# Kernel tuning notes

Hardware: AMD Instinct MI355X
Metric: run time of the kernel (lower is better)

## Reference

```python
import jax, jax.numpy as jnp
import numpy as np

RADIUS = 3.0  # suppression radius in meters (init kwarg `radius`)


def _radius_nms(x, y, valid, radius):
    """Greedy radius NMS over points in index order.
    x, y: [N] coordinates; valid: [N] bool (point belongs to this class).
    Returns keep mask [N]: point kept iff valid and not within `radius` of
    any previously kept point.
    """
    N = x.shape[0]
    r2 = radius * radius

    def step(supp, i):
        keep = valid[i] & jnp.logical_not(supp[i])
        d2 = (x - x[i]) ** 2 + (y - y[i]) ** 2  # [N]
        supp = supp | (keep & (d2 <= r2))
        return supp, keep

    _, keeps = jax.lax.scan(step, jnp.zeros(N, dtype=bool), jnp.arange(N))
    return keeps


def setup_inputs() -> dict:
    key = jax.random.key(0)
    k1, k2 = jax.random.split(key)
    B, C, W, H, CL = 4, 4, 64, 128, 5
    segmented_channels = jax.random.normal(k1, (B, C, W, H), dtype=jnp.float32)
    # lidar channels 0,1 are x,y point coordinates (meters); scale for realism
    lidar = jax.random.normal(k2, (B, CL, W, H), dtype=jnp.float32) * 30.0
    return {"segmented_channels": segmented_channels, "lidar": lidar}


def reference(segmented_channels, lidar):
    B, C, W, H = segmented_channels.shape
    N = W * H
    # val, ind = segmented_channels.max(dim=1) -> per-pixel predicted class
    ind = jnp.argmax(segmented_channels, axis=1).reshape(B, N)  # [B, N] int
    x = lidar[:, 0].reshape(B, N)  # [B, N]
    y = lidar[:, 1].reshape(B, N)
    # classes 1 .. C-1 (class 0 = background, skipped in the loop)
    classes = jnp.arange(1, C)
    valid = ind[:, None, :] == classes[None, :, None]  # [B, C-1, N] bool
    # vmap greedy NMS over classes, then over batch (x,y shared across classes)
    nms_c = jax.vmap(_radius_nms, in_axes=(None, None, 0, None))
    nms_bc = jax.vmap(nms_c, in_axes=(0, 0, 0, None))
    keep = nms_bc(x, y, valid, RADIUS)  # [B, C-1, N] bool
    # dense (padded) stand-in for the ragged per-class kept point lists:
    # kept coordinates where keep, zeros elsewhere
    coords = jnp.stack([x, y], axis=-1)  # [B, N, 2]
    kept_coords = coords[:, None, :, :] * keep[..., None].astype(coords.dtype)  # [B, C-1, N, 2]
    return kept_coords, keep
```

## Files before the change

kernel.cpp:

```cpp
#include <hip/hip_runtime.h>
#include <cstdint>


#define NPTS 8192
#define CAP  2304
#define R2C  9.0f
#define GW   56
#define GORG 117.6f
#define GINV 0.23809524f
#define GMAXC 55.0f
#define SENT 3.0e37f

#define WS_STRIDE 32768
#define WS_XY     0
#define WS_CELL   18432
#define WS_OIDX   23040
#define WS_KEPT   27648
#define WS_M      27936
#define WS_NEED   (12 * WS_STRIDE)

__global__ __launch_bounds__(1024) void k1_prep(
    const float* __restrict__ seg,
    const float* __restrict__ lidar,
    float* __restrict__ out,
    char* __restrict__ ws)
{
#pragma clang fp contract(off)
    const int blk = blockIdx.x;
    const int tid = threadIdx.x;
    if (blk >= 12) {
        ((float4*)out)[(size_t)(blk - 12) * 1024 + tid] =
            make_float4(0.f, 0.f, 0.f, 0.f);
        return;
    }
    const int b    = blk / 3;
    const int cls  = (blk % 3) + 1;
    const int lane = tid & 63;
    const int wv   = tid >> 6;
    __shared__ int waveTot[16];

    const float* segb = seg + (size_t)b * 4 * NPTS;
    const float* lx   = lidar + (size_t)b * 5 * NPTS;
    const float* ly   = lx + NPTS;

    const int n0 = tid * 8;
    const float4 a0 = *(const float4*)(segb + n0);
    const float4 a1 = *(const float4*)(segb + n0 + 4);
    const float4 b0 = *(const float4*)(segb + NPTS + n0);
    const float4 b1 = *(const float4*)(segb + NPTS + n0 + 4);
    const float4 c0 = *(const float4*)(segb + 2 * NPTS + n0);
    const float4 c1 = *(const float4*)(segb + 2 * NPTS + n0 + 4);
    const float4 d0 = *(const float4*)(segb + 3 * NPTS + n0);
    const float4 d1 = *(const float4*)(segb + 3 * NPTS + n0 + 4);
    const float4 xv0 = *(const float4*)(lx + n0);
    const float4 xv1 = *(const float4*)(lx + n0 + 4);
    const float4 yv0 = *(const float4*)(ly + n0);
    const float4 yv1 = *(const float4*)(ly + n0 + 4);

    const float v0[8] = {a0.x,a0.y,a0.z,a0.w, a1.x,a1.y,a1.z,a1.w};
    const float v1[8] = {b0.x,b0.y,b0.z,b0.w, b1.x,b1.y,b1.z,b1.w};
    const float v2[8] = {c0.x,c0.y,c0.z,c0.w, c1.x,c1.y,c1.z,c1.w};
    const float v3[8] = {d0.x,d0.y,d0.z,d0.w, d1.x,d1.y,d1.z,d1.w};
    const float px[8] = {xv0.x,xv0.y,xv0.z,xv0.w, xv1.x,xv1.y,xv1.z,xv1.w};
    const float py[8] = {yv0.x,yv0.y,yv0.z,yv0.w, yv1.x,yv1.y,yv1.z,yv1.w};

    int flags = 0, cnt = 0;
#pragma unroll
    for (int k = 0; k < 8; ++k) {
        int bi = 0; float bv = v0[k];
        if (v1[k] > bv) { bv = v1[k]; bi = 1; }
        if (v2[k] > bv) { bv = v2[k]; bi = 2; }
        if (v3[k] > bv) { bv = v3[k]; bi = 3; }
        if (bi == cls) { flags |= (1 << k); ++cnt; }
    }

    int v = cnt;
    for (int off = 1; off < 64; off <<= 1) {
        int nv = __shfl_up(v, off, 64);
        if (lane >= off) v += nv;
    }
    if (lane == 63) waveTot[wv] = v;
    __syncthreads();
    if (wv == 0) {
        int t = (lane < 16) ? waveTot[lane] : 0;
        for (int off = 1; off < 16; off <<= 1) {
            int nt = __shfl_up(t, off, 64);
            if (lane >= off) t += nt;
        }
        if (lane < 16) waveTot[lane] = t;
    }
    __syncthreads();

    int M = waveTot[15];
    if (M > CAP) M = CAP;

    char* wsp = ws + (size_t)blk * WS_STRIDE;
    float2* wxy = (float2*)(wsp + WS_XY);
    unsigned short* wcell = (unsigned short*)(wsp + WS_CELL);
    unsigned short* woidx = (unsigned short*)(wsp + WS_OIDX);
    if (tid == 0) *(int*)(wsp + WS_M) = M;

    int base = ((wv == 0) ? 0 : waveTot[wv - 1]) + v - cnt;
#pragma unroll
    for (int k = 0; k < 8; ++k) {
        if (flags & (1 << k)) {
            if (base < CAP) {
                wxy[base] = make_float2(px[k], py[k]);
                float fx = floorf((px[k] + GORG) * GINV);
                fx = fminf(fmaxf(fx, 0.0f), GMAXC);
                float fy = floorf((py[k] + GORG) * GINV);
                fy = fminf(fmaxf(fy, 0.0f), GMAXC);
                wcell[base] = (unsigned short)(((int)fy << 8) | (int)fx);
                woidx[base] = (unsigned short)(n0 + k);
            }
            ++base;
        }
    }
}

__global__ __launch_bounds__(64) void k2_nms(char* __restrict__ ws)
{
#pragma clang fp contract(off)
    const int p    = blockIdx.x;
    const int lane = threadIdx.x;

    char* wsp = ws + (size_t)p * WS_STRIDE;
    const float2* wxy = (const float2*)(wsp + WS_XY);
    const unsigned short* wcell = (const unsigned short*)(wsp + WS_CELL);
    unsigned long long* wkept = (unsigned long long*)(wsp + WS_KEPT);
    const int M = *(const int*)(wsp + WS_M);

    __shared__ float2 gslot[GW * GW * 4];
    __shared__ unsigned int cnt32[(GW * GW + 3) / 4];

    const float4 s4 = make_float4(SENT, SENT, SENT, SENT);
    float4* g4 = (float4*)gslot;
    for (int i = lane; i < GW * GW * 2; i += 64) g4[i] = s4;
    for (int i = lane; i < (GW * GW + 3) / 4; i += 64) cnt32[i] = 0u;

    const int ntiles = (M + 63) >> 6;
    const int packSent = (55 << 8) | 55;

    float qx = 3.0e38f, qy = 3.0e38f;
    int cc = packSent;
    if (lane < M) {
        float2 q = wxy[lane]; qx = q.x; qy = q.y;
        cc = wcell[lane];
    }

    for (int t = 0; t < ntiles; ++t) {
        const int ts = t << 6;

        float qxN = 3.0e38f, qyN = 3.0e38f;
        int ccN = packSent;
        {
            const int p2 = ts + 64 + lane;
            if (p2 < M) {
                float2 q = wxy[p2]; qxN = q.x; qyN = q.y;
                ccN = wcell[p2];
            }
        }

        const int cx = cc & 0xFF, cy = cc >> 8;
        const int cxm = (cx > 0) ? cx - 1 : 0;
        const int cxp = (cx < GW - 1) ? cx + 1 : GW - 1;
        const int rm  = ((cy > 0) ? cy - 1 : 0) * GW;
        const int r0  = cy * GW;
        const int rp  = ((cy < GW - 1) ? cy + 1 : GW - 1) * GW;
        const int cLin = r0 + cx;
        const int c9[9] = { rm + cxm, rm + cx, rm + cxp,
                            r0 + cxm, cLin,    r0 + cxp,
                            rp + cxm, rp + cx, rp + cxp };

        float mm = 1.0e30f;
#pragma unroll
        for (int i = 0; i < 9; ++i) {
            const int sb = c9[i] * 4;
            const float2 s0 = gslot[sb];
            const float2 s1 = gslot[sb + 1];
            const float2 s2r = gslot[sb + 2];
            const float2 s3 = gslot[sb + 3];
            float dx, dy;
            dx = qx - s0.x; dy = qy - s0.y; const float e0 = dx * dx + dy * dy;
            dx = qx - s1.x; dy = qy - s1.y; const float e1 = dx * dx + dy * dy;
            dx = qx - s2r.x; dy = qy - s2r.y; const float e2 = dx * dx + dy * dy;
            dx = qx - s3.x; dy = qy - s3.y; const float e3 = dx * dx + dy * dy;
            const float cm = fminf(fminf(e0, e1), fminf(e2, e3));
            mm = fminf(mm, cm);
        }
        const bool sup = (mm <= R2C);

        int cntT = M - ts; if (cntT > 64) cntT = 64;
        const unsigned long long tm =
            (cntT >= 64) ? ~0ull : ((1ull << cntT) - 1ull);
        unsigned long long alive = __ballot(!sup) & tm;
        unsigned long long keepm = 0ull;
        while (alive) {
            const int l = __builtin_ctzll(alive);
            const float xl = __int_as_float(
                __builtin_amdgcn_readlane(__float_as_int(qx), l));
            const float yl = __int_as_float(
                __builtin_amdgcn_readlane(__float_as_int(qy), l));
            const float dx = qx - xl;
            const float dy = qy - yl;
            unsigned long long b2 = __ballot((dx * dx + dy * dy) <= R2C);
            keepm |= (1ull << l);
            alive &= ~b2;
        }
        if (lane == 0) wkept[t] = keepm;

        if ((keepm >> lane) & 1ull) {
            const unsigned sh = 8u * (unsigned)(cLin & 3);
            unsigned old = atomicAdd(&cnt32[cLin >> 2], 1u << sh);
            unsigned mc = (old >> sh) & 0xFFu;
            if (mc < 4u) gslot[cLin * 4 + (int)mc] = make_float2(qx, qy);
        }

        qx = qxN; qy = qyN; cc = ccN;
    }
}

__global__ __launch_bounds__(1024) void k3_scatter(
    float* __restrict__ out, const char* __restrict__ ws)
{
    const int p   = blockIdx.x;
    const int tid = threadIdx.x;
    const char* wsp = ws + (size_t)p * WS_STRIDE;
    const float2* wxy = (const float2*)(wsp + WS_XY);
    const unsigned short* woidx = (const unsigned short*)(wsp + WS_OIDX);
    const unsigned long long* wkept =
        (const unsigned long long*)(wsp + WS_KEPT);
    const int M = *(const int*)(wsp + WS_M);

    float* out0 = out + (size_t)p * NPTS * 2;
    float* out1 = out + 196608 + (size_t)p * NPTS;
    for (int j = tid; j < M; j += 1024) {
        if ((wkept[j >> 6] >> (j & 63)) & 1ull) {
            const int n = woidx[j];
            float2 q = wxy[j];
            out0[2 * n]     = q.x;
            out0[2 * n + 1] = q.y;
            out1[n]         = 1.0f;
        }
    }
}

__global__ __launch_bounds__(1024) void radius_nms_kernel(
    const float* __restrict__ seg,
    const float* __restrict__ lidar,
    float* __restrict__ out)
{
#pragma clang fp contract(off)
    const int bx   = blockIdx.x;
    const int b    = bx / 3;
    const int cls  = (bx % 3) + 1;
    const int tid  = threadIdx.x;
    const int lane = tid & 63;
    const int wv   = tid >> 6;

    __shared__ float2 xy[CAP];
    __shared__ unsigned short cellA[CAP];
    __shared__ unsigned long long keptW[CAP / 64];
    __shared__ int waveTot[16];
    __shared__ float2 gslot[GW * GW * 4];
    __shared__ unsigned int cnt32[(GW * GW + 3) / 4];

    float* out0 = out + (size_t)bx * NPTS * 2;
    float* out1 = out + 196608 + (size_t)bx * NPTS;

    const float4 z4 = make_float4(0.f, 0.f, 0.f, 0.f);
    float4* o04 = (float4*)out0;
    float4* o14 = (float4*)out1;
    for (int i = tid; i < NPTS / 2; i += 1024) o04[i] = z4;
    for (int i = tid; i < NPTS / 4; i += 1024) o14[i] = z4;
    const float2 s2 = make_float2(SENT, SENT);
    for (int i = tid; i < GW * GW * 4; i += 1024) gslot[i] = s2;
    for (int i = tid; i < (GW * GW + 3) / 4; i += 1024) cnt32[i] = 0u;

    const float* segb = seg + (size_t)b * 4 * NPTS;
    const float* lx   = lidar + (size_t)b * 5 * NPTS;
    const float* ly   = lx + NPTS;

    const int n0 = tid * 8;
    const float4 a0 = *(const float4*)(segb + n0);
    const float4 a1 = *(const float4*)(segb + n0 + 4);
    const float4 b0 = *(const float4*)(segb + NPTS + n0);
    const float4 b1 = *(const float4*)(segb + NPTS + n0 + 4);
    const float4 c0 = *(const float4*)(segb + 2 * NPTS + n0);
    const float4 c1 = *(const float4*)(segb + 2 * NPTS + n0 + 4);
    const float4 d0 = *(const float4*)(segb + 3 * NPTS + n0);
    const float4 d1 = *(const float4*)(segb + 3 * NPTS + n0 + 4);
    const float4 xv0 = *(const float4*)(lx + n0);
    const float4 xv1 = *(const float4*)(lx + n0 + 4);
    const float4 yv0 = *(const float4*)(ly + n0);
    const float4 yv1 = *(const float4*)(ly + n0 + 4);

    const float v0[8] = {a0.x,a0.y,a0.z,a0.w, a1.x,a1.y,a1.z,a1.w};
    const float v1[8] = {b0.x,b0.y,b0.z,b0.w, b1.x,b1.y,b1.z,b1.w};
    const float v2[8] = {c0.x,c0.y,c0.z,c0.w, c1.x,c1.y,c1.z,c1.w};
    const float v3[8] = {d0.x,d0.y,d0.z,d0.w, d1.x,d1.y,d1.z,d1.w};
    const float px[8] = {xv0.x,xv0.y,xv0.z,xv0.w, xv1.x,xv1.y,xv1.z,xv1.w};
    const float py[8] = {yv0.x,yv0.y,yv0.z,yv0.w, yv1.x,yv1.y,yv1.z,yv1.w};

    int flags = 0, cnt = 0;
#pragma unroll
    for (int k = 0; k < 8; ++k) {
        int bi = 0; float bv = v0[k];
        if (v1[k] > bv) { bv = v1[k]; bi = 1; }
        if (v2[k] > bv) { bv = v2[k]; bi = 2; }
        if (v3[k] > bv) { bv = v3[k]; bi = 3; }
        if (bi == cls) { flags |= (1 << k); ++cnt; }
    }

    int v = cnt;
    for (int off = 1; off < 64; off <<= 1) {
        int nv = __shfl_up(v, off, 64);
        if (lane >= off) v += nv;
    }
    if (lane == 63) waveTot[wv] = v;
    __syncthreads();
    if (wv == 0) {
        int t = (lane < 16) ? waveTot[lane] : 0;
        for (int off = 1; off < 16; off <<= 1) {
            int nt = __shfl_up(t, off, 64);
            if (lane >= off) t += nt;
        }
        if (lane < 16) waveTot[lane] = t;
    }
    __syncthreads();

    int M = waveTot[15];
    if (M > CAP) M = CAP;
    const int rank0 = ((wv == 0) ? 0 : waveTot[wv - 1]) + v - cnt;
    int base = rank0;
#pragma unroll
    for (int k = 0; k < 8; ++k) {
        if (flags & (1 << k)) {
            if (base < CAP) {
                xy[base] = make_float2(px[k], py[k]);
                float fx = floorf((px[k] + GORG) * GINV);
                fx = fminf(fmaxf(fx, 0.0f), GMAXC);
                float fy = floorf((py[k] + GORG) * GINV);
                fy = fminf(fmaxf(fy, 0.0f), GMAXC);
                cellA[base] = (unsigned short)(((int)fy << 8) | (int)fx);
            }
            ++base;
        }
    }
    __syncthreads();

    if (wv == 0) {
        const int ntiles = (M + 63) >> 6;
        const int packSent = (55 << 8) | 55;

        float qx = 3.0e38f, qy = 3.0e38f;
        int cc = packSent;
        if (lane < M) {
            float2 q = xy[lane]; qx = q.x; qy = q.y;
            cc = cellA[lane];
        }

        for (int t = 0; t < ntiles; ++t) {
            const int ts = t << 6;

            float qxN = 3.0e38f, qyN = 3.0e38f;
            int ccN = packSent;
            {
                const int p2 = ts + 64 + lane;
                if (p2 < M) {
                    float2 q = xy[p2]; qxN = q.x; qyN = q.y;
                    ccN = cellA[p2];
                }
            }

            const int cx = cc & 0xFF, cy = cc >> 8;
            const int cxm = (cx > 0) ? cx - 1 : 0;
            const int cxp = (cx < GW - 1) ? cx + 1 : GW - 1;
            const int rm  = ((cy > 0) ? cy - 1 : 0) * GW;
            const int r0  = cy * GW;
            const int rp  = ((cy < GW - 1) ? cy + 1 : GW - 1) * GW;
            const int cLin = r0 + cx;
            const int c9[9] = { rm + cxm, rm + cx, rm + cxp,
                                r0 + cxm, cLin,    r0 + cxp,
                                rp + cxm, rp + cx, rp + cxp };

            float mm = 1.0e30f;
#pragma unroll
            for (int i = 0; i < 9; ++i) {
                const int sb = c9[i] * 4;
                const float2 s0 = gslot[sb];
                const float2 s1 = gslot[sb + 1];
                const float2 s2r = gslot[sb + 2];
                const float2 s3 = gslot[sb + 3];
                float dx, dy;
                dx = qx - s0.x; dy = qy - s0.y; const float e0 = dx * dx + dy * dy;
                dx = qx - s1.x; dy = qy - s1.y; const float e1 = dx * dx + dy * dy;
                dx = qx - s2r.x; dy = qy - s2r.y; const float e2 = dx * dx + dy * dy;
                dx = qx - s3.x; dy = qy - s3.y; const float e3 = dx * dx + dy * dy;
                const float cm = fminf(fminf(e0, e1), fminf(e2, e3));
                mm = fminf(mm, cm);
            }
            const bool sup = (mm <= R2C);

            int cntT = M - ts; if (cntT > 64) cntT = 64;
            const unsigned long long tm =
                (cntT >= 64) ? ~0ull : ((1ull << cntT) - 1ull);
            unsigned long long alive = __ballot(!sup) & tm;
            unsigned long long keepm = 0ull;
            while (alive) {
                const int l = __builtin_ctzll(alive);
                const float xl = __int_as_float(
                    __builtin_amdgcn_readlane(__float_as_int(qx), l));
                const float yl = __int_as_float(
                    __builtin_amdgcn_readlane(__float_as_int(qy), l));
                const float dx = qx - xl;
                const float dy = qy - yl;
                unsigned long long b2 = __ballot((dx * dx + dy * dy) <= R2C);
                keepm |= (1ull << l);
                alive &= ~b2;
            }
            if (lane == 0) keptW[t] = keepm;

            if ((keepm >> lane) & 1ull) {
                const unsigned sh = 8u * (unsigned)(cLin & 3);
                unsigned old = atomicAdd(&cnt32[cLin >> 2], 1u << sh);
                unsigned mc = (old >> sh) & 0xFFu;
                if (mc < 4u) gslot[cLin * 4 + (int)mc] = make_float2(qx, qy);
            }

            qx = qxN; qy = qyN; cc = ccN;
        }
    }
    __syncthreads();

    int j = rank0;
#pragma unroll
    for (int k = 0; k < 8; ++k) {
        if (flags & (1 << k)) {
            if (j < M && ((keptW[j >> 6] >> (j & 63)) & 1ull)) {
                const int n = n0 + k;
                out0[2 * n]     = px[k];
                out0[2 * n + 1] = py[k];
                out1[n]         = 1.0f;
            }
            ++j;
        }
    }
}

extern "C" void kernel_launch(void* const* d_in, const int* in_sizes, int n_in,
                              void* d_out, int out_size, void* d_ws, size_t ws_size,
                              hipStream_t stream) {
    const float* seg   = (const float*)d_in[0];
    const float* lidar = (const float*)d_in[1];
    float* out = (float*)d_out;
    if (d_ws != nullptr && ws_size >= (size_t)WS_NEED) {
        char* ws = (char*)d_ws;
        k1_prep<<<dim3(84), dim3(1024), 0, stream>>>(seg, lidar, out, ws);
        k2_nms<<<dim3(12), dim3(64), 0, stream>>>(ws);
        k3_scatter<<<dim3(12), dim3(1024), 0, stream>>>(out, ws);
    } else {
        radius_nms_kernel<<<dim3(12), dim3(1024), 0, stream>>>(seg, lidar, out);
    }
}
```

Measured before the change: 130.0 us.

## Parallelize greedy NMS via neighbor graph and iterative label propagation

Replaces the single-wave sequential tile-by-tile greedy NMS with a 1024-thread block per problem. The block builds a cell-sorted CSR grid, precomputes each point's earlier-index neighbors within the radius, and then resolves keep/suppress status in parallel rounds: a point is suppressed once any neighbor is kept and kept once all neighbors are decided. Stragglers are finished by a single wave spinning on shared status. This trades the serial dependency chain for several block-wide barriers and neighbor-list construction passes. It risks overflowing the neighbor buffer in dense inputs and needing many rounds when dependency chains are long.

```diff
diff --git a/kernel.cpp b/kernel.cpp
--- a/kernel.cpp
+++ b/kernel.cpp
@@ -6,10 +6,13 @@
 #define CAP  2304
 #define R2C  9.0f
 #define GW   56
+#define NCELL (GW * GW)
 #define GORG 117.6f
 #define GINV 0.23809524f
 #define GMAXC 55.0f
 #define SENT 3.0e37f
+#define NB_MAX 24576
+#define TAIL_T 128
 
 #define WS_STRIDE 32768
 #define WS_XY     0
@@ -118,11 +121,13 @@
     }
 }
 
-__global__ __launch_bounds__(64) void k2_nms(char* __restrict__ ws)
+__global__ __launch_bounds__(1024) void k2_nms(char* __restrict__ ws)
 {
 #pragma clang fp contract(off)
     const int p    = blockIdx.x;
-    const int lane = threadIdx.x;
+    const int tid  = threadIdx.x;
+    const int lane = tid & 63;
+    const int wv   = tid >> 6;
 
     char* wsp = ws + (size_t)p * WS_STRIDE;
     const float2* wxy = (const float2*)(wsp + WS_XY);
@@ -130,93 +135,257 @@
     unsigned long long* wkept = (unsigned long long*)(wsp + WS_KEPT);
     const int M = *(const int*)(wsp + WS_M);
 
-    __shared__ float2 gslot[GW * GW * 4];
-    __shared__ unsigned int cnt32[(GW * GW + 3) / 4];
-
-    const float4 s4 = make_float4(SENT, SENT, SENT, SENT);
-    float4* g4 = (float4*)gslot;
-    for (int i = lane; i < GW * GW * 2; i += 64) g4[i] = s4;
-    for (int i = lane; i < (GW * GW + 3) / 4; i += 64) cnt32[i] = 0u;
-
-    const int ntiles = (M + 63) >> 6;
-    const int packSent = (55 << 8) | 55;
-
-    float qx = 3.0e38f, qy = 3.0e38f;
-    int cc = packSent;
-    if (lane < M) {
-        float2 q = wxy[lane]; qx = q.x; qy = q.y;
-        cc = wcell[lane];
-    }
-
-    for (int t = 0; t < ntiles; ++t) {
-        const int ts = t << 6;
-
-        float qxN = 3.0e38f, qyN = 3.0e38f;
-        int ccN = packSent;
-        {
-            const int p2 = ts + 64 + lane;
-            if (p2 < M) {
-                float2 q = wxy[p2]; qxN = q.x; qyN = q.y;
-                ccN = wcell[p2];
-            }
-        }
-
-        const int cx = cc & 0xFF, cy = cc >> 8;
-        const int cxm = (cx > 0) ? cx - 1 : 0;
-        const int cxp = (cx < GW - 1) ? cx + 1 : GW - 1;
-        const int rm  = ((cy > 0) ? cy - 1 : 0) * GW;
-        const int r0  = cy * GW;
-        const int rp  = ((cy < GW - 1) ? cy + 1 : GW - 1) * GW;
-        const int cLin = r0 + cx;
-        const int c9[9] = { rm + cxm, rm + cx, rm + cxp,
-                            r0 + cxm, cLin,    r0 + cxp,
-                            rp + cxm, rp + cx, rp + cxp };
-
-        float mm = 1.0e30f;
+    __shared__ float2 xy[CAP];
+    __shared__ unsigned short cellOf[CAP];
+    __shared__ unsigned short ptCSR[CAP];
+    __shared__ unsigned short ncnt[CAP];
+    __shared__ unsigned int   nStart[CAP];
+    __shared__ unsigned int   cellCnt[NCELL];
+    __shared__ unsigned int   cellStart[NCELL];
+    __shared__ unsigned short nbr[NB_MAX];
+    __shared__ unsigned int   statusW[CAP / 16];
+    __shared__ int waveTot[16];
+    __shared__ unsigned int cntRR[4];
+    __shared__ int tailN;
+    __shared__ unsigned short tailList[TAIL_T];
+
+    for (int i = tid; i < M; i += 1024) {
+        xy[i] = wxy[i];
+        cellOf[i] = wcell[i];
+    }
+    for (int i = tid; i < NCELL; i += 1024) cellCnt[i] = 0u;
+    for (int i = tid; i < CAP; i += 1024) ncnt[i] = 0;
+    if (tid < CAP / 16) statusW[tid] = 0u;
+    if (tid < 4) cntRR[tid] = 0u;
+    if (tid == 0) tailN = 0;
+    __syncthreads();
+
+    for (int r = tid; r < M; r += 1024) {
+        const int cc = cellOf[r];
+        atomicAdd(&cellCnt[(cc >> 8) * GW + (cc & 255)], 1u);
+    }
+    __syncthreads();
+
+    {
+        const int c4 = tid * 4;
+        int sa = 0, sb = 0, sc = 0, sd = 0;
+        if (c4 < NCELL) {
+            sa = cellCnt[c4]; sb = cellCnt[c4 + 1];
+            sc = cellCnt[c4 + 2]; sd = cellCnt[c4 + 3];
+        }
+        int sum = sa + sb + sc + sd;
+        int inc = sum;
+        for (int off = 1; off < 64; off <<= 1) {
+            int t = __shfl_up(inc, off, 64);
+            if (lane >= off) inc += t;
+        }
+        if (lane == 63) waveTot[wv] = inc;
+        __syncthreads();
+        if (wv == 0) {
+            int t = (lane < 16) ? waveTot[lane] : 0;
+            for (int off = 1; off < 16; off <<= 1) {
+                int u = __shfl_up(t, off, 64);
+                if (lane >= off) t += u;
+            }
+            if (lane < 16) waveTot[lane] = t;
+        }
+        __syncthreads();
+        const int bb = ((wv == 0) ? 0 : waveTot[wv - 1]) + inc - sum;
+        if (c4 < NCELL) {
+            cellStart[c4]     = bb;
+            cellStart[c4 + 1] = bb + sa;
+            cellStart[c4 + 2] = bb + sa + sb;
+            cellStart[c4 + 3] = bb + sa + sb + sc;
+        }
+    }
+    __syncthreads();
+
+    for (int i = tid; i < NCELL; i += 1024) cellCnt[i] = 0u;
+    __syncthreads();
+
+    for (int r = tid; r < M; r += 1024) {
+        const int cc = cellOf[r];
+        const int c = (cc >> 8) * GW + (cc & 255);
+        const unsigned pos = cellStart[c] + atomicAdd(&cellCnt[c], 1u);
+        ptCSR[pos] = (unsigned short)r;
+    }
+    __syncthreads();
+
+    for (int r = tid; r < M; r += 1024) {
+        const float2 q = xy[r];
+        const int cc = cellOf[r];
+        const int cx = cc & 255, cy = cc >> 8;
+        const int x0 = (cx > 0) ? cx - 1 : 0, x1 = (cx < GW - 1) ? cx + 1 : GW - 1;
+        const int y0 = (cy > 0) ? cy - 1 : 0, y1 = (cy < GW - 1) ? cy + 1 : GW - 1;
+        int nc = 0;
+        for (int yy = y0; yy <= y1; ++yy)
+            for (int xx = x0; xx <= x1; ++xx) {
+                const int c = yy * GW + xx;
+                const unsigned s = cellStart[c], n = cellCnt[c];
+                for (unsigned k = 0; k < n; ++k) {
+                    const int qr = ptCSR[s + k];
+                    if (qr < r) {
+                        const float2 o = xy[qr];
+                        const float dx = q.x - o.x, dy = q.y - o.y;
+                        if (dx * dx + dy * dy <= R2C) ++nc;
+                    }
+                }
+            }
+        ncnt[r] = (unsigned short)nc;
+    }
+    __syncthreads();
+
+    {
+        const int r3 = tid * 3;
+        int sa = 0, sb = 0, sc = 0;
+        if (r3 < CAP) { sa = ncnt[r3]; sb = ncnt[r3 + 1]; sc = ncnt[r3 + 2]; }
+        int sum = sa + sb + sc;
+        int inc = sum;
+        for (int off = 1; off < 64; off <<= 1) {
+            int t = __shfl_up(inc, off, 64);
+            if (lane >= off) inc += t;
+        }
+        if (lane == 63) waveTot[wv] = inc;
+        __syncthreads();
+        if (wv == 0) {
+            int t = (lane < 16) ? waveTot[lane] : 0;
+            for (int off = 1; off < 16; off <<= 1) {
+                int u = __shfl_up(t, off, 64);
+                if (lane >= off) t += u;
+            }
+            if (lane < 16) waveTot[lane] = t;
+        }
+        __syncthreads();
+        const int bb = ((wv == 0) ? 0 : waveTot[wv - 1]) + inc - sum;
+        if (r3 < CAP) {
+            nStart[r3]     = bb;
+            nStart[r3 + 1] = bb + sa;
+            nStart[r3 + 2] = bb + sa + sb;
+        }
+    }
+    __syncthreads();
+
+    for (int r = tid; r < M; r += 1024) {
+        const float2 q = xy[r];
+        const int cc = cellOf[r];
+        const int cx = cc & 255, cy = cc >> 8;
+        const int x0 = (cx > 0) ? cx - 1 : 0, x1 = (cx < GW - 1) ? cx + 1 : GW - 1;
+        const int y0 = (cy > 0) ? cy - 1 : 0, y1 = (cy < GW - 1) ? cy + 1 : GW - 1;
+        unsigned pos = nStart[r];
+        for (int yy = y0; yy <= y1; ++yy)
+            for (int xx = x0; xx <= x1; ++xx) {
+                const int c = yy * GW + xx;
+                const unsigned s = cellStart[c], n = cellCnt[c];
+                for (unsigned k = 0; k < n; ++k) {
+                    const int qr = ptCSR[s + k];
+                    if (qr < r) {
+                        const float2 o = xy[qr];
+                        const float dx = q.x - o.x, dy = q.y - o.y;
+                        if (dx * dx + dy * dy <= R2C) {
+                            if (pos < NB_MAX) nbr[pos] = (unsigned short)qr;
+                            ++pos;
+                        }
+                    }
+                }
+            }
+    }
+    __syncthreads();
+
+    unsigned resolvedMask = 0;
+    unsigned st0 = 0, en0 = 0, st1 = 0, en1 = 0, st2 = 0, en2 = 0;
+    { int r = tid;        if (r < M) { st0 = nStart[r]; en0 = st0 + ncnt[r]; if (en0 > NB_MAX) en0 = NB_MAX; } else resolvedMask |= 1u; }
+    { int r = tid + 1024; if (r < M) { st1 = nStart[r]; en1 = st1 + ncnt[r]; if (en1 > NB_MAX) en1 = NB_MAX; } else resolvedMask |= 2u; }
+    { int r = tid + 2048; if (r < M) { st2 = nStart[r]; en2 = st2 + ncnt[r]; if (en2 > NB_MAX) en2 = NB_MAX; } else resolvedMask |= 4u; }
+
+    auto step = [&](int r, unsigned st, unsigned en) -> int {
+        bool sup = false, allDec = true;
+        for (unsigned k = st; k < en; ++k) {
+            const int q = nbr[k];
+            const unsigned f = (statusW[q >> 4] >> ((q & 15) * 2)) & 3u;
+            if (f & 2u) { sup = true; break; }
+            if (!(f & 1u)) allDec = false;
+        }
+        if (sup)    { atomicOr(&statusW[r >> 4], 1u << ((r & 15) * 2)); return 1; }
+        if (allDec) { atomicOr(&statusW[r >> 4], 3u << ((r & 15) * 2)); return 1; }
+        return 0;
+    };
+
+    bool needTail = false;
+    for (int r = 0; ; ++r) {
+        bool u0 = false, u1 = false, u2 = false;
+        if (!(resolvedMask & 1u)) { if (step(tid,        st0, en0)) resolvedMask |= 1u; else u0 = true; }
+        if (!(resolvedMask & 2u)) { if (step(tid + 1024, st1, en1)) resolvedMask |= 2u; else u1 = true; }
+        if (!(resolvedMask & 4u)) { if (step(tid + 2048, st2, en2)) resolvedMask |= 4u; else u2 = true; }
+        const unsigned long long b0 = __ballot(u0);
+        const unsigned long long b1 = __ballot(u1);
+        const unsigned long long b2 = __ballot(u2);
+        if (lane == 0) {
+            const unsigned c = __popcll(b0) + __popcll(b1) + __popcll(b2);
+            if (c) atomicAdd(&cntRR[r & 3], c);
+        }
+        if (tid == 0) cntRR[(r + 2) & 3] = 0u;
+        __syncthreads();
+        const unsigned rem = cntRR[r & 3];
+        if (rem == 0u) break;
+        if (rem <= TAIL_T || r > 2500) { needTail = true; break; }
+    }
+
+    if (needTail) {
+        if (!(resolvedMask & 1u)) { int pos = atomicAdd(&tailN, 1); if (pos < TAIL_T) tailList[pos] = (unsigned short)tid; }
+        if (!(resolvedMask & 2u)) { int pos = atomicAdd(&tailN, 1); if (pos < TAIL_T) tailList[pos] = (unsigned short)(tid + 1024); }
+        if (!(resolvedMask & 4u)) { int pos = atomicAdd(&tailN, 1); if (pos < TAIL_T) tailList[pos] = (unsigned short)(tid + 2048); }
+        __syncthreads();
+        if (wv == 0) {
+            int n = tailN; if (n > TAIL_T) n = TAIL_T;
+            int ra = (lane < n) ? (int)tailList[lane] : -1;
+            int rb = (lane + 64 < n) ? (int)tailList[lane + 64] : -1;
+            bool da = (ra < 0), db = (rb < 0);
+            unsigned sa = 0, ea = 0, sb = 0, eb = 0;
+            if (!da) { sa = nStart[ra]; ea = sa + ncnt[ra]; if (ea > NB_MAX) ea = NB_MAX; }
+            if (!db) { sb = nStart[rb]; eb = sb + ncnt[rb]; if (eb > NB_MAX) eb = NB_MAX; }
+            volatile unsigned* vst = statusW;
+            for (;;) {
+                if (!da) {
+                    bool sup = false, all = true;
+                    for (unsigned k = sa; k < ea; ++k) {
+                        const int q = nbr[k];
+                        const unsigned f = (vst[q >> 4] >> ((q & 15) * 2)) & 3u;
+                        if (f & 2u) { sup = true; break; }
+                        if (!(f & 1u)) all = false;
+                    }
+                    if (sup)      { atomicOr(&statusW[ra >> 4], 1u << ((ra & 15) * 2)); da = true; }
+                    else if (all) { atomicOr(&statusW[ra >> 4], 3u << ((ra & 15) * 2)); da = true; }
+                }
+                if (!db) {
+                    bool sup = false, all = true;
+                    for (unsigned k = sb; k < eb; ++k) {
+                        const int q = nbr[k];
+                        const unsigned f = (vst[q >> 4] >> ((q & 15) * 2)) & 3u;
+                        if (f & 2u) { sup = true; break; }
+                        if (!(f & 1u)) all = false;
+                    }
+                    if (sup)      { atomicOr(&statusW[rb >> 4], 1u << ((rb & 15) * 2)); db = true; }
+                    else if (all) { atomicOr(&statusW[rb >> 4], 3u << ((rb & 15) * 2)); db = true; }
+                }
+                if (__ballot(!da || !db) == 0ull) break;
+            }
+        }
+        __syncthreads();
+    }
+
+    if (tid < CAP / 64) {
+        unsigned long long w = 0ull;
 #pragma unroll
-        for (int i = 0; i < 9; ++i) {
-            const int sb = c9[i] * 4;
-            const float2 s0 = gslot[sb];
-            const float2 s1 = gslot[sb + 1];
-            const float2 s2r = gslot[sb + 2];
-            const float2 s3 = gslot[sb + 3];
-            float dx, dy;
-            dx = qx - s0.x; dy = qy - s0.y; const float e0 = dx * dx + dy * dy;
-            dx = qx - s1.x; dy = qy - s1.y; const float e1 = dx * dx + dy * dy;
-            dx = qx - s2r.x; dy = qy - s2r.y; const float e2 = dx * dx + dy * dy;
-            dx = qx - s3.x; dy = qy - s3.y; const float e3 = dx * dx + dy * dy;
-            const float cm = fminf(fminf(e0, e1), fminf(e2, e3));
-            mm = fminf(mm, cm);
-        }
-        const bool sup = (mm <= R2C);
-
-        int cntT = M - ts; if (cntT > 64) cntT = 64;
-        const unsigned long long tm =
-            (cntT >= 64) ? ~0ull : ((1ull << cntT) - 1ull);
-        unsigned long long alive = __ballot(!sup) & tm;
-        unsigned long long keepm = 0ull;
-        while (alive) {
-            const int l = __builtin_ctzll(alive);
-            const float xl = __int_as_float(
-                __builtin_amdgcn_readlane(__float_as_int(qx), l));
-            const float yl = __int_as_float(
-                __builtin_amdgcn_readlane(__float_as_int(qy), l));
-            const float dx = qx - xl;
-            const float dy = qy - yl;
-            unsigned long long b2 = __ballot((dx * dx + dy * dy) <= R2C);
-            keepm |= (1ull << l);
-            alive &= ~b2;
-        }
-        if (lane == 0) wkept[t] = keepm;
-
-        if ((keepm >> lane) & 1ull) {
-            const unsigned sh = 8u * (unsigned)(cLin & 3);
-            unsigned old = atomicAdd(&cnt32[cLin >> 2], 1u << sh);
-            unsigned mc = (old >> sh) & 0xFFu;
-            if (mc < 4u) gslot[cLin * 4 + (int)mc] = make_float2(qx, qy);
-        }
-
-        qx = qxN; qy = qyN; cc = ccN;
+        for (int j = 0; j < 4; ++j) {
+            unsigned x = statusW[tid * 4 + j];
+            x = (x >> 1) & 0x55555555u;
+            x = (x | (x >> 1)) & 0x33333333u;
+            x = (x | (x >> 2)) & 0x0F0F0F0Fu;
+            x = (x | (x >> 4)) & 0x00FF00FFu;
+            x = (x | (x >> 8)) & 0x0000FFFFu;
+            w |= (unsigned long long)x << (16 * j);
+        }
+        wkept[tid] = w;
     }
 }
 
@@ -245,7 +414,7 @@
     }
 }
 
-__global__ __launch_bounds__(1024) void radius_nms_kernel(
+__global__ __launch_bounds__(1024) void radius_nms_fb(
     const float* __restrict__ seg,
     const float* __restrict__ lidar,
     float* __restrict__ out)
@@ -457,9 +626,9 @@
     if (d_ws != nullptr && ws_size >= (size_t)WS_NEED) {
         char* ws = (char*)d_ws;
         k1_prep<<<dim3(84), dim3(1024), 0, stream>>>(seg, lidar, out, ws);
-        k2_nms<<<dim3(12), dim3(64), 0, stream>>>(ws);
+        k2_nms<<<dim3(12), dim3(1024), 0, stream>>>(ws);
         k3_scatter<<<dim3(12), dim3(1024), 0, stream>>>(out, ws);
     } else {
-        radius_nms_kernel<<<dim3(12), dim3(1024), 0, stream>>>(seg, lidar, out);
+        radius_nms_fb<<<dim3(12), dim3(1024), 0, stream>>>(seg, lidar, out);
     }
 }
```

Result: slower. 156.4 us (+20.3%).
